# Kernel tuning notes

Hardware: AMD Instinct MI355X
Metric: run time of the kernel (lower is better)

Reference implementation:

```python
import jax, jax.numpy as jnp
import numpy as np

PIXELS_PER_CELL = (8, 8)
CELLS_PER_BLOCK = (2, 2)
ORIENTATIONS = 9
GRAY_W = jnp.array([0.2125, 0.7154, 0.0721], dtype=jnp.float32)  # skimage rgb2gray
EPS = 1e-5  # skimage L2-Hys eps


def setup_inputs() -> dict:
    key = jax.random.key(0)
    x = jax.random.uniform(key, (64, 512, 512, 3), dtype=jnp.float32)
    return {"x": x}


def _hog(x):
    # rgb2gray
    gray = jnp.einsum("bhwc,c->bhw", x, GRAY_W)  # [B,H,W]
    B, H, W = gray.shape
    pr, pc = PIXELS_PER_CELL
    br, bc = CELLS_PER_BLOCK
    O = ORIENTATIONS

    # skimage _hog_channel_gradient: central differences, zero at borders
    g_row = jnp.zeros_like(gray).at[:, 1:-1, :].set(gray[:, 2:, :] - gray[:, :-2, :])
    g_col = jnp.zeros_like(gray).at[:, :, 1:-1].set(gray[:, :, 2:] - gray[:, :, :-2])

    mag = jnp.hypot(g_row, g_col)
    ori = jnp.rad2deg(jnp.arctan2(g_row, g_col)) % 180.0  # unsigned orientation

    ncr, ncc = H // pr, W // pc
    mag = mag[:, : ncr * pr, : ncc * pc]
    ori = ori[:, : ncr * pr, : ncc * pc]

    spacing = 180.0 / O
    cell_area = float(pr * pc)
    # per-orientation-bin cell histograms: hard binning (skimage cell_hog)
    hists = []
    for o in range(O):
        lo, hi = spacing * o, spacing * (o + 1)
        contrib = jnp.where((ori >= lo) & (ori < hi), mag, 0.0)
        # sum over each pr x pc cell, divide by cell area
        h = contrib.reshape(B, ncr, pr, ncc, pc).sum(axis=(2, 4)) / cell_area
        hists.append(h)
    hist = jnp.stack(hists, axis=-1)  # [B, ncr, ncc, O]

    # overlapping blocks of cells, stride 1 cell
    nbr, nbc = ncr - br + 1, ncc - bc + 1
    block = jnp.stack(
        [jnp.stack([hist[:, r : r + nbr, c : c + nbc, :] for c in range(bc)], axis=3)
         for r in range(br)], axis=3)  # [B, nbr, nbc, br, bc, O]

    # L2-Hys normalization (skimage default block_norm)
    norm = jnp.sqrt(jnp.sum(block * block, axis=(3, 4, 5), keepdims=True) + EPS ** 2)
    blk = jnp.minimum(block / norm, 0.2)
    norm2 = jnp.sqrt(jnp.sum(blk * blk, axis=(3, 4, 5), keepdims=True) + EPS ** 2)
    blk = blk / norm2

    return blk.reshape(B, -1).astype(jnp.float32)


def reference(x):
    return _hog(x)
```

## Files before the change

kernel.cpp:

```cpp
#include <hip/hip_runtime.h>
#include <math.h>

#define IMG_H 512
#define IMG_W 512
#define NCELL 64
#define NORI 9

__device__ __forceinline__ float fdlibm_atanf_inl(float x) {
#pragma clang fp contract(off)
    const float one = 1.0f;
    int hx = __float_as_int(x);
    int ix = hx & 0x7fffffff;
    int id;
    if (ix >= 0x4c800000) {
        const float v = 1.5707962513e+00f + 7.5497894159e-08f;
        return (hx > 0) ? v : -v;
    }
    if (ix < 0x3ee00000) {
        if (ix < 0x39800000) return x;
        id = -1;
    } else {
        x = fabsf(x);
        if (ix < 0x3f980000) {
            if (ix < 0x3f300000) { id = 0; x = (2.0f * x - one) / (2.0f + x); }
            else                 { id = 1; x = (x - one) / (x + one); }
        } else {
            if (ix < 0x401c0000) { id = 2; x = (x - 1.5f) / (one + 1.5f * x); }
            else                 { id = 3; x = -1.0f / x; }
        }
    }
    float z = x * x;
    float w = z * z;
    float s1 = z * (3.3333334327e-01f + w * (1.4285714924e-01f + w * (9.0908870101e-02f
             + w * (6.6610731184e-02f + w * (4.9768779427e-02f + w * 1.6285819933e-02f)))));
    float s2 = w * (-2.0000000298e-01f + w * (-1.1111110449e-01f + w * (-7.6918758452e-02f
             + w * (-5.8335702866e-02f + w * -3.6531571299e-02f))));
    if (id < 0) return x - x * (s1 + s2);
    const float hi = (id == 0) ? 4.6364760399e-01f : (id == 1) ? 7.8539812565e-01f
                   : (id == 2) ? 9.8279368877e-01f : 1.5707962513e+00f;
    const float lo = (id == 0) ? 5.0121582440e-09f : (id == 1) ? 3.7748947079e-08f
                   : (id == 2) ? 3.4473217170e-08f : 7.5497894159e-08f;
    z = hi - ((x * (s1 + s2) - lo) - x);
    return (hx < 0) ? -z : z;
}

__device__ __forceinline__ int fdlibm_bin_inl(float y, float x) {
#pragma clang fp contract(off)
    const float tiny   = 1.0e-30f;
    const float pi_o_2 = 1.5707963705e+00f;
    const float pi     = 3.1415927410e+00f;
    const float pi_lo  = -8.7422776573e-08f;

    int hx = __float_as_int(x), ix = hx & 0x7fffffff;
    int hy = __float_as_int(y), iy = hy & 0x7fffffff;
    float th;
    if (hx == 0x3f800000) { th = fdlibm_atanf_inl(y); }
    else {
        int m = ((hy >> 31) & 1) | ((hx >> 30) & 2);
        if (iy == 0) {
            switch (m) {
                case 0:
                case 1: th = y; break;
                case 2: th =  pi + tiny; break;
                default: th = -pi - tiny; break;
            }
        } else if (ix == 0) {
            th = (hy < 0) ? -pi_o_2 - tiny : pi_o_2 + tiny;
        } else {
            int k = (iy - ix) >> 23;
            float z;
            int mm = m;
            if (k > 26) {
                z = pi_o_2 + 0.5f * pi_lo;
                mm &= 1;
            } else if (k < -26 && hx < 0) {
                z = 0.0f;
            } else {
                z = fdlibm_atanf_inl(fabsf(y / x));
            }
            switch (mm) {
                case 0:  th = z; break;
                case 1:  th = -z; break;
                case 2:  th = pi - (z - pi_lo); break;
                default: th = (z - pi_lo) - pi; break;
            }
        }
    }
    const float RAD2DEG = (float)(180.0 / 3.14159265358979311600e+00);
    float m = fmodf(th * RAD2DEG, 180.0f);
    if (m < 0.0f) m += 180.0f;
    int o = (int)(m * 0.05f);
    if (o < 9) {
        if (m < 20.0f * (float)o) --o;
        else if (m >= 20.0f * (float)(o + 1)) ++o;
    }
    return o;
}

__global__ __launch_bounds__(512, 6) void hog_hist_kernel(const float* __restrict__ x,
                                                          float* __restrict__ hist) {
#pragma clang fp contract(off)
    const int bid = blockIdx.x;
    const int b   = bid >> 6;
    const int cr  = bid & 63;
    const int t   = threadIdx.x;
    const int h0  = cr * 8;

    __shared__ __align__(16) float g[10][IMG_W];

    const float GW0 = 0.2125f, GW1 = 0.7154f, GW2 = 0.0721f;
    float4 A[3], C[3], D[3];
#pragma unroll
    for (int k = 0; k < 3; ++k) {
        const int gi = t + 512 * k;
        if (k < 2 || t < 256) {
            const int rr = gi >> 7;
            int h = h0 - 1 + rr;
            if (h < 0)   h = 1;
            if (h > 511) h = 510;
            const int grp = gi & 127;
            const float4* p4 = (const float4*)x + (size_t)(b * IMG_H + h) * (IMG_W * 3 / 4)
                               + (size_t)grp * 3;
            A[k] = p4[0]; C[k] = p4[1]; D[k] = p4[2];
        }
    }
#pragma unroll
    for (int k = 0; k < 3; ++k) {
        const int gi = t + 512 * k;
        if (k < 2 || t < 256) {
            const int rr = gi >> 7;
            const int wg = (gi & 127) * 4;
            float4 gv;
            gv.x = __builtin_fmaf(A[k].z, GW2, __builtin_fmaf(A[k].y, GW1, A[k].x * GW0));
            gv.y = __builtin_fmaf(C[k].y, GW2, __builtin_fmaf(C[k].x, GW1, A[k].w * GW0));
            gv.z = __builtin_fmaf(D[k].x, GW2, __builtin_fmaf(C[k].w, GW1, C[k].z * GW0));
            gv.w = __builtin_fmaf(D[k].w, GW2, __builtin_fmaf(D[k].z, GW1, D[k].y * GW0));
            *(float4*)&g[rr][wg] = gv;
        }
    }
    __syncthreads();

    const int w   = t;
    const int wl  = (w == 0)   ? 0   : w - 1;
    const int wr  = (w == 511) ? 511 : w + 1;
    const bool wok = (w >= 1) && (w <= 510);
    const int c   = w >> 3;
    const int jl  = t & 7;

    float cc[10], ee[8], ww[8];
#pragma unroll
    for (int i = 0; i < 10; ++i) cc[i] = g[i][w];
#pragma unroll
    for (int i = 0; i < 8; ++i) { ee[i] = g[i + 1][wr]; ww[i] = g[i + 1][wl]; }

    const float CK[8] = { 0.9396926208f,  0.7660444431f,  0.5f,            0.1736481777f,
                         -0.1736481777f, -0.5f,           -0.7660444431f, -0.9396926208f };
    const float SK[8] = { 0.3420201433f,  0.6427876097f,  0.8660254038f,  0.9848077530f,
                          0.9848077530f,  0.8660254038f,  0.6427876097f,  0.3420201433f };

    float bh[9];
#pragma unroll
    for (int k = 0; k < 9; ++k) bh[k] = 0.0f;

#pragma unroll
    for (int r = 0; r < 8; ++r) {
        const float gr = cc[r + 2] - cc[r];
        const float gc = wok ? (ee[r] - ww[r]) : 0.0f;
        const float mag = __builtin_amdgcn_sqrtf(__builtin_fmaf(gr, gr, gc * gc));

        const float gy = fabsf(gr);
        const float gx = (gr < 0.0f) ? -gc : gc;
        const float th = 1e-4f * mag;
        int  o = 0;
        bool suspect = false;
#pragma unroll
        for (int k = 0; k < 8; ++k) {
            const float ck = __builtin_fmaf(gy, CK[k], -(gx * SK[k]));
            o += (ck >= 0.0f) ? 1 : 0;
            suspect = suspect || (fabsf(ck) < th);
        }
        suspect = suspect || ((gx < 0.0f) && (gy < 1e-5f * fabsf(gc)));
        if (gy == 0.0f) { o = 0; suspect = false; }
        if (__builtin_expect(suspect, 0)) {
            o = fdlibm_bin_inl(gr, gc);
        }
#pragma unroll
        for (int k = 0; k < 9; ++k) bh[k] += (o == k) ? mag : 0.0f;
    }

#pragma unroll
    for (int k = 0; k < 9; ++k) {
        bh[k] += __shfl_xor(bh[k], 1, 64);
        bh[k] += __shfl_xor(bh[k], 2, 64);
        bh[k] += __shfl_xor(bh[k], 4, 64);
    }
    float mv = bh[0];
#pragma unroll
    for (int k = 1; k < 8; ++k) mv = (jl == k) ? bh[k] : mv;
    float* hout = hist + (size_t)(b * NCELL + cr) * (NCELL * NORI);
    hout[c * NORI + jl] = mv * 0.015625f;
    if (jl == 0) hout[c * NORI + 8] = bh[8] * 0.015625f;
}

__global__ __launch_bounds__(256) void hog_norm_kernel(const float* __restrict__ hist,
                                                       float* __restrict__ out) {
#pragma clang fp contract(off)
    const int bid = blockIdx.x;
    const int b   = bid / 63;
    const int r   = bid % 63;
    const int t   = threadIdx.x;
    const int c   = t >> 2;
    const int l   = t & 3;
    if (c >= 63) return;

    const int bi = l >> 1, bj = l & 1;
    const float* v = hist + ((size_t)(b * NCELL + r + bi) * NCELL + (c + bj)) * NORI;

    float vv[9];
    float ss = 0.0f;
#pragma unroll
    for (int k = 0; k < 9; ++k) { vv[k] = v[k]; ss += vv[k] * vv[k]; }
    ss += __shfl_xor(ss, 1, 64);
    ss += __shfl_xor(ss, 2, 64);
    const float rn1 = 1.0f / sqrtf(ss + 1e-10f);
    float ss2 = 0.0f;
#pragma unroll
    for (int k = 0; k < 9; ++k) { vv[k] = fminf(vv[k] * rn1, 0.2f); ss2 += vv[k] * vv[k]; }
    ss2 += __shfl_xor(ss2, 1, 64);
    ss2 += __shfl_xor(ss2, 2, 64);
    const float rn2 = 1.0f / sqrtf(ss2 + 1e-10f);

    float* od = out + (size_t)bid * (63 * 36) + (c * 36 + l * 9);
#pragma unroll
    for (int k = 0; k < 9; ++k) od[k] = vv[k] * rn2;
}

extern "C" void kernel_launch(void* const* d_in, const int* in_sizes, int n_in,
                              void* d_out, int out_size, void* d_ws, size_t ws_size,
                              hipStream_t stream) {
    const float* x = (const float*)d_in[0];
    float* out     = (float*)d_out;
    float* hist    = (float*)d_ws;

    hog_hist_kernel<<<dim3(64 * 64), dim3(512), 0, stream>>>(x, hist);
    hog_norm_kernel<<<dim3(64 * 63), dim3(256), 0, stream>>>(hist, out);
}
```

Measured before the change: 296.8 us.

## Restructure histogram kernel to one wave per cell row with register row streaming

Replaces the shared-memory tile (one 512-thread block per cell row) with one 64-lane wave per cell row, where each lane owns a whole 8-pixel cell. Rows are streamed through registers with a rolling three-row window and a one-row prefetch, and horizontal neighbours come from wave shuffles. This drops LDS traffic, the block barrier and the cross-lane histogram reduction. In exchange each lane issues wider strided loads (six float4s per row, 96-byte stride across lanes), the grid is four times smaller, and per-thread register pressure rises.

```diff
diff --git a/kernel.cpp b/kernel.cpp
--- a/kernel.cpp
+++ b/kernel.cpp
@@ -97,61 +97,56 @@
     return o;
 }
 
-__global__ __launch_bounds__(512, 6) void hog_hist_kernel(const float* __restrict__ x,
+__device__ __forceinline__ void cvt8(const float4 R[6], float g[8]) {
+#pragma clang fp contract(off)
+    const float GW0 = 0.2125f, GW1 = 0.7154f, GW2 = 0.0721f;
+    g[0] = __builtin_fmaf(R[0].z, GW2, __builtin_fmaf(R[0].y, GW1, R[0].x * GW0));
+    g[1] = __builtin_fmaf(R[1].y, GW2, __builtin_fmaf(R[1].x, GW1, R[0].w * GW0));
+    g[2] = __builtin_fmaf(R[2].x, GW2, __builtin_fmaf(R[1].w, GW1, R[1].z * GW0));
+    g[3] = __builtin_fmaf(R[2].w, GW2, __builtin_fmaf(R[2].z, GW1, R[2].y * GW0));
+    g[4] = __builtin_fmaf(R[3].z, GW2, __builtin_fmaf(R[3].y, GW1, R[3].x * GW0));
+    g[5] = __builtin_fmaf(R[4].y, GW2, __builtin_fmaf(R[4].x, GW1, R[3].w * GW0));
+    g[6] = __builtin_fmaf(R[5].x, GW2, __builtin_fmaf(R[4].w, GW1, R[4].z * GW0));
+    g[7] = __builtin_fmaf(R[5].w, GW2, __builtin_fmaf(R[5].z, GW1, R[5].y * GW0));
+}
+
+__global__ __launch_bounds__(256, 4) void hog_hist_kernel(const float* __restrict__ x,
                                                           float* __restrict__ hist) {
 #pragma clang fp contract(off)
-    const int bid = blockIdx.x;
-    const int b   = bid >> 6;
-    const int cr  = bid & 63;
-    const int t   = threadIdx.x;
-    const int h0  = cr * 8;
-
-    __shared__ __align__(16) float g[10][IMG_W];
-
-    const float GW0 = 0.2125f, GW1 = 0.7154f, GW2 = 0.0721f;
-    float4 A[3], C[3], D[3];
-#pragma unroll
-    for (int k = 0; k < 3; ++k) {
-        const int gi = t + 512 * k;
-        if (k < 2 || t < 256) {
-            const int rr = gi >> 7;
-            int h = h0 - 1 + rr;
-            if (h < 0)   h = 1;
-            if (h > 511) h = 510;
-            const int grp = gi & 127;
-            const float4* p4 = (const float4*)x + (size_t)(b * IMG_H + h) * (IMG_W * 3 / 4)
-                               + (size_t)grp * 3;
-            A[k] = p4[0]; C[k] = p4[1]; D[k] = p4[2];
-        }
-    }
-#pragma unroll
-    for (int k = 0; k < 3; ++k) {
-        const int gi = t + 512 * k;
-        if (k < 2 || t < 256) {
-            const int rr = gi >> 7;
-            const int wg = (gi & 127) * 4;
-            float4 gv;
-            gv.x = __builtin_fmaf(A[k].z, GW2, __builtin_fmaf(A[k].y, GW1, A[k].x * GW0));
-            gv.y = __builtin_fmaf(C[k].y, GW2, __builtin_fmaf(C[k].x, GW1, A[k].w * GW0));
-            gv.z = __builtin_fmaf(D[k].x, GW2, __builtin_fmaf(C[k].w, GW1, C[k].z * GW0));
-            gv.w = __builtin_fmaf(D[k].w, GW2, __builtin_fmaf(D[k].z, GW1, D[k].y * GW0));
-            *(float4*)&g[rr][wg] = gv;
-        }
-    }
-    __syncthreads();
-
-    const int w   = t;
-    const int wl  = (w == 0)   ? 0   : w - 1;
-    const int wr  = (w == 511) ? 511 : w + 1;
-    const bool wok = (w >= 1) && (w <= 510);
-    const int c   = w >> 3;
-    const int jl  = t & 7;
-
-    float cc[10], ee[8], ww[8];
-#pragma unroll
-    for (int i = 0; i < 10; ++i) cc[i] = g[i][w];
-#pragma unroll
-    for (int i = 0; i < 8; ++i) { ee[i] = g[i + 1][wr]; ww[i] = g[i + 1][wl]; }
+    const int bid  = blockIdx.x;
+    const int b    = bid >> 4;
+    const int s    = bid & 15;
+    const int q    = threadIdx.x >> 6;
+    const int lane = threadIdx.x & 63;
+    const int cr   = s * 4 + q;
+    const int h0   = cr * 8;
+
+    const float4* X4 = (const float4*)x + (size_t)b * (IMG_H * (IMG_W * 3 / 4));
+
+    auto rowp = [&](int h) -> const float4* {
+        if (h < 0)   h = 1;
+        if (h > 511) h = 510;
+        return X4 + (size_t)h * (IMG_W * 3 / 4) + lane * 6;
+    };
+
+    float gp[8], gm[8], gn[8];
+    {
+        float4 R0[6], R1[6];
+        const float4* p0 = rowp(h0 - 1);
+        const float4* p1 = rowp(h0);
+#pragma unroll
+        for (int i = 0; i < 6; ++i) R0[i] = p0[i];
+#pragma unroll
+        for (int i = 0; i < 6; ++i) R1[i] = p1[i];
+        cvt8(R0, gp);
+        cvt8(R1, gm);
+    }
+    float4 P[6];
+    {
+        const float4* p = rowp(h0 + 1);
+#pragma unroll
+        for (int i = 0; i < 6; ++i) P[i] = p[i];
+    }
 
     const float CK[8] = { 0.9396926208f,  0.7660444431f,  0.5f,            0.1736481777f,
                          -0.1736481777f, -0.5f,           -0.7660444431f, -0.9396926208f };
@@ -163,43 +158,63 @@
     for (int k = 0; k < 9; ++k) bh[k] = 0.0f;
 
 #pragma unroll
-    for (int r = 0; r < 8; ++r) {
-        const float gr = cc[r + 2] - cc[r];
-        const float gc = wok ? (ee[r] - ww[r]) : 0.0f;
-        const float mag = __builtin_amdgcn_sqrtf(__builtin_fmaf(gr, gr, gc * gc));
-
-        const float gy = fabsf(gr);
-        const float gx = (gr < 0.0f) ? -gc : gc;
-        const float th = 1e-4f * mag;
-        int  o = 0;
-        bool suspect = false;
-#pragma unroll
-        for (int k = 0; k < 8; ++k) {
-            const float ck = __builtin_fmaf(gy, CK[k], -(gx * SK[k]));
-            o += (ck >= 0.0f) ? 1 : 0;
-            suspect = suspect || (fabsf(ck) < th);
-        }
-        suspect = suspect || ((gx < 0.0f) && (gy < 1e-5f * fabsf(gc)));
-        if (gy == 0.0f) { o = 0; suspect = false; }
-        if (__builtin_expect(suspect, 0)) {
-            o = fdlibm_bin_inl(gr, gc);
-        }
-#pragma unroll
-        for (int k = 0; k < 9; ++k) bh[k] += (o == k) ? mag : 0.0f;
-    }
-
-#pragma unroll
-    for (int k = 0; k < 9; ++k) {
-        bh[k] += __shfl_xor(bh[k], 1, 64);
-        bh[k] += __shfl_xor(bh[k], 2, 64);
-        bh[k] += __shfl_xor(bh[k], 4, 64);
-    }
-    float mv = bh[0];
-#pragma unroll
-    for (int k = 1; k < 8; ++k) mv = (jl == k) ? bh[k] : mv;
-    float* hout = hist + (size_t)(b * NCELL + cr) * (NCELL * NORI);
-    hout[c * NORI + jl] = mv * 0.015625f;
-    if (jl == 0) hout[c * NORI + 8] = bh[8] * 0.015625f;
+    for (int j8 = 0; j8 < 8; ++j8) {
+        const int h = h0 + j8;
+
+        float4 N[6];
+        const bool pf = (j8 < 7);
+        if (pf) {
+            const float4* p = rowp(h + 2);
+#pragma unroll
+            for (int i = 0; i < 6; ++i) N[i] = p[i];
+        }
+
+        cvt8(P, gn);
+
+        const float glft = __shfl_up(gm[7], 1, 64);
+        const float grgt = __shfl_down(gm[0], 1, 64);
+
+#pragma unroll
+        for (int j = 0; j < 8; ++j) {
+            const int  w   = lane * 8 + j;
+            const bool wok = (w >= 1) && (w <= 510);
+            const float left  = (j == 0) ? glft : gm[j - 1];
+            const float right = (j == 7) ? grgt : gm[j + 1];
+            const float gr = gn[j] - gp[j];
+            const float gc = wok ? (right - left) : 0.0f;
+            const float mag = __builtin_amdgcn_sqrtf(__builtin_fmaf(gr, gr, gc * gc));
+
+            const float gy = fabsf(gr);
+            const float gx = (gr < 0.0f) ? -gc : gc;
+            const float th = 1e-4f * mag;
+            int  o = 0;
+            bool suspect = false;
+#pragma unroll
+            for (int k = 0; k < 8; ++k) {
+                const float ck = __builtin_fmaf(gy, CK[k], -(gx * SK[k]));
+                o += (ck >= 0.0f) ? 1 : 0;
+                suspect = suspect || (fabsf(ck) < th);
+            }
+            suspect = suspect || ((gx < 0.0f) && (gy < 1e-5f * fabsf(gc)));
+            if (gy == 0.0f) { o = 0; suspect = false; }
+            if (__builtin_expect(suspect, 0)) {
+                o = fdlibm_bin_inl(gr, gc);
+            }
+#pragma unroll
+            for (int k = 0; k < 9; ++k) bh[k] += (o == k) ? mag : 0.0f;
+        }
+
+#pragma unroll
+        for (int k = 0; k < 8; ++k) { gp[k] = gm[k]; gm[k] = gn[k]; }
+        if (pf) {
+#pragma unroll
+            for (int i = 0; i < 6; ++i) P[i] = N[i];
+        }
+    }
+
+    float* hout = hist + ((size_t)(b * NCELL + cr) * NCELL + lane) * NORI;
+#pragma unroll
+    for (int k = 0; k < 9; ++k) hout[k] = bh[k] * 0.015625f;
 }
 
 __global__ __launch_bounds__(256) void hog_norm_kernel(const float* __restrict__ hist,
@@ -242,6 +257,6 @@
     float* out     = (float*)d_out;
     float* hist    = (float*)d_ws;
 
-    hog_hist_kernel<<<dim3(64 * 64), dim3(512), 0, stream>>>(x, hist);
+    hog_hist_kernel<<<dim3(64 * 16), dim3(256), 0, stream>>>(x, hist);
     hog_norm_kernel<<<dim3(64 * 63), dim3(256), 0, stream>>>(hist, out);
 }
```

New measurement: 310.6 us. 4.7% more time.

## Stage RGB rows through LDS and defer rare fdlibm atan2 fallback

Applied to the files above, without the earlier changes.

The load phase now copies the 10 input rows (two passes of 5 rows) into a shared raw buffer with coalesced float4 loads, then converts to grayscale by reading interleaved RGB from LDS, instead of each thread loading three float4s directly. The rare exact-atan2 fallback is moved out of the unrolled row loop: up to two suspect pixels are recorded and resolved afterwards, with a recompute loop for more. This aims to cut divergence and register pressure inside the hot loop, at the cost of an extra 30KB of LDS per block, which may lower occupancy, and two extra barriers.

```diff
diff --git a/kernel.cpp b/kernel.cpp
--- a/kernel.cpp
+++ b/kernel.cpp
@@ -106,39 +106,32 @@
     const int t   = threadIdx.x;
     const int h0  = cr * 8;
 
-    __shared__ __align__(16) float g[10][IMG_W];
+    __shared__ __align__(16) float4 raw[1920];
+    __shared__ __align__(16) float  g[10][IMG_W];
 
     const float GW0 = 0.2125f, GW1 = 0.7154f, GW2 = 0.0721f;
-    float4 A[3], C[3], D[3];
-#pragma unroll
-    for (int k = 0; k < 3; ++k) {
-        const int gi = t + 512 * k;
-        if (k < 2 || t < 256) {
-            const int rr = gi >> 7;
-            int h = h0 - 1 + rr;
+
+#pragma unroll
+    for (int p = 0; p < 2; ++p) {
+        for (int i = t; i < 1920; i += 512) {
+            const int rr  = i / 384;
+            const int idx = i - rr * 384;
+            int h = h0 - 1 + p * 5 + rr;
             if (h < 0)   h = 1;
             if (h > 511) h = 510;
-            const int grp = gi & 127;
-            const float4* p4 = (const float4*)x + (size_t)(b * IMG_H + h) * (IMG_W * 3 / 4)
-                               + (size_t)grp * 3;
-            A[k] = p4[0]; C[k] = p4[1]; D[k] = p4[2];
-        }
-    }
-#pragma unroll
-    for (int k = 0; k < 3; ++k) {
-        const int gi = t + 512 * k;
-        if (k < 2 || t < 256) {
-            const int rr = gi >> 7;
-            const int wg = (gi & 127) * 4;
-            float4 gv;
-            gv.x = __builtin_fmaf(A[k].z, GW2, __builtin_fmaf(A[k].y, GW1, A[k].x * GW0));
-            gv.y = __builtin_fmaf(C[k].y, GW2, __builtin_fmaf(C[k].x, GW1, A[k].w * GW0));
-            gv.z = __builtin_fmaf(D[k].x, GW2, __builtin_fmaf(C[k].w, GW1, C[k].z * GW0));
-            gv.w = __builtin_fmaf(D[k].w, GW2, __builtin_fmaf(D[k].z, GW1, D[k].y * GW0));
-            *(float4*)&g[rr][wg] = gv;
-        }
-    }
-    __syncthreads();
+            raw[i] = ((const float4*)x)[(size_t)(b * IMG_H + h) * 384 + idx];
+        }
+        __syncthreads();
+        const float* rf = (const float*)raw;
+#pragma unroll
+        for (int k = 0; k < 5; ++k) {
+            const float r_ = rf[k * 1536 + 3 * t + 0];
+            const float g_ = rf[k * 1536 + 3 * t + 1];
+            const float b_ = rf[k * 1536 + 3 * t + 2];
+            g[p * 5 + k][t] = __builtin_fmaf(b_, GW2, __builtin_fmaf(g_, GW1, r_ * GW0));
+        }
+        __syncthreads();
+    }
 
     const int w   = t;
     const int wl  = (w == 0)   ? 0   : w - 1;
@@ -162,6 +155,10 @@
 #pragma unroll
     for (int k = 0; k < 9; ++k) bh[k] = 0.0f;
 
+    int   nsus = 0;
+    float s0gr = 0.0f, s0gc = 0.0f, s0mag = 0.0f;
+    float s1gr = 0.0f, s1gc = 0.0f, s1mag = 0.0f;
+
 #pragma unroll
     for (int r = 0; r < 8; ++r) {
         const float gr = cc[r + 2] - cc[r];
@@ -182,10 +179,46 @@
         suspect = suspect || ((gx < 0.0f) && (gy < 1e-5f * fabsf(gc)));
         if (gy == 0.0f) { o = 0; suspect = false; }
         if (__builtin_expect(suspect, 0)) {
-            o = fdlibm_bin_inl(gr, gc);
+            if (nsus == 0)      { s0gr = gr; s0gc = gc; s0mag = mag; }
+            else if (nsus == 1) { s1gr = gr; s1gc = gc; s1mag = mag; }
+            ++nsus;
+            o = 9;
         }
 #pragma unroll
         for (int k = 0; k < 9; ++k) bh[k] += (o == k) ? mag : 0.0f;
+    }
+
+    if (__builtin_expect(nsus > 0, 0)) {
+        if (nsus <= 2) {
+            {
+                const int o = fdlibm_bin_inl(s0gr, s0gc);
+                if (o < 9) bh[o] += s0mag;
+            }
+            if (nsus == 2) {
+                const int o = fdlibm_bin_inl(s1gr, s1gc);
+                if (o < 9) bh[o] += s1mag;
+            }
+        } else {
+            for (int r = 0; r < 8; ++r) {
+                const float gr = g[r + 2][w] - g[r][w];
+                const float gc = wok ? (g[r + 1][wr] - g[r + 1][wl]) : 0.0f;
+                const float mag = __builtin_amdgcn_sqrtf(__builtin_fmaf(gr, gr, gc * gc));
+                const float gy = fabsf(gr);
+                const float gx = (gr < 0.0f) ? -gc : gc;
+                const float th = 1e-4f * mag;
+                bool suspect = false;
+                for (int k = 0; k < 8; ++k) {
+                    const float ck = __builtin_fmaf(gy, CK[k], -(gx * SK[k]));
+                    suspect = suspect || (fabsf(ck) < th);
+                }
+                suspect = suspect || ((gx < 0.0f) && (gy < 1e-5f * fabsf(gc)));
+                if (gy == 0.0f) suspect = false;
+                if (suspect) {
+                    const int o = fdlibm_bin_inl(gr, gc);
+                    if (o < 9) bh[o] += mag;
+                }
+            }
+        }
     }
 
 #pragma unroll
```

New measurement: 310.2 us. +4.5%, slower.
